# Performance work log

Measured on AMD Instinct MI355X. Metric: run time of the kernel, lower is better.

Reference implementation:

```python
import jax, jax.numpy as jnp
from jax import lax
import numpy as np

N, M, P, K = 2, 16384, 5023, 4
C_PLANE, HP = 32, 256
OUT_DIM = 32


def _harmonic(x):
    # pytorch3d HarmonicEmbedding(n=4, logspace, omega_0=1, append_input=True)
    f = jnp.asarray([1.0, 2.0, 4.0, 8.0], x.dtype)
    e = (x[..., None] * f).reshape(x.shape[:-1] + (-1,))  # [..., 12]
    return jnp.concatenate([jnp.sin(e), jnp.cos(e), x], axis=-1)  # [..., 27]


def _grid_sample2d(img, grid):
    # img [C,H,W], grid [M,2] (x->W, y->H) in [-1,1]; bilinear, zero pad, align_corners=False
    C, H, W = img.shape
    x = (grid[:, 0] + 1.0) * (W / 2.0) - 0.5
    y = (grid[:, 1] + 1.0) * (H / 2.0) - 0.5
    x0 = jnp.floor(x); y0 = jnp.floor(y)
    x1 = x0 + 1.0; y1 = y0 + 1.0
    wx1 = x - x0; wx0 = 1.0 - wx1
    wy1 = y - y0; wy0 = 1.0 - wy1
    def gather(ix, iy):
        valid = ((ix >= 0) & (ix < W) & (iy >= 0) & (iy < H)).astype(img.dtype)
        ixc = jnp.clip(ix, 0, W - 1).astype(jnp.int32)
        iyc = jnp.clip(iy, 0, H - 1).astype(jnp.int32)
        return img[:, iyc, ixc] * valid[None, :]  # [C,M]
    out = (gather(x0, y0) * (wx0 * wy0) + gather(x1, y0) * (wx1 * wy0)
           + gather(x0, y1) * (wx0 * wy1) + gather(x1, y1) * (wx1 * wy1))
    return out.T  # [M,C]


def _forward(coordinates, directions, points_position, tex_tplanes, emb_table,
             pw1, pb1, pw2, pb2, fw1, fb1, fw2, fb2, fw3, fb3, dw, db, rw1, rb1, rw2, rb2):
    c = coordinates
    p = points_position
    # --- triplane sampling (EG3D projections (x,y),(x,z),(z,x)), mean over planes ---
    proj = jnp.stack([c[..., :2],
                      c[..., jnp.array([0, 2])],
                      c[..., jnp.array([2, 0])]], axis=1)  # [N,3,M,2]
    tex = jax.vmap(jax.vmap(_grid_sample2d))(tex_tplanes, proj).mean(axis=1)  # [N,M,32]
    # --- KNN (squared distances, ascending, as pytorch3d knn_points) ---
    d2 = (jnp.sum(c * c, -1)[:, :, None] + jnp.sum(p * p, -1)[:, None, :]
          - 2.0 * jnp.einsum('nmc,npc->nmp', c, p))  # [N,M,P]
    negd, idx = lax.top_k(-d2, K)
    dist = -negd  # [N,M,K]
    nn = jax.vmap(lambda pts, i: pts[i])(p, idx)  # [N,M,K,3]
    pf = emb_table[idx]  # [N,M,K,32]
    rel = c[:, :, None, :] - nn
    rel = rel / jnp.maximum(jnp.linalg.norm(rel, axis=-1, keepdims=True), 1e-12)
    h = jnp.concatenate([pf, _harmonic(rel)], axis=-1)  # [N,M,K,59]
    h = jax.nn.relu(h @ pw1 + pb1) @ pw2 + pb2  # [N,M,K,32]
    w = 1.0 / dist
    w = w / jnp.sum(w, axis=1, keepdims=True)  # dim=1 exactly as in source
    pts_feat = jnp.sum(h * w[..., None], axis=2)  # [N,M,32]
    # --- dense MLP stack ---
    feat = jnp.concatenate([tex, pts_feat], axis=-1)  # [N,M,64]
    feat = jax.nn.relu(feat @ fw1 + fb1)
    feat = jax.nn.relu(feat @ fw2 + fb2)
    feat = feat @ fw3 + fb3  # [N,M,128]
    selector = jnp.all((c > -1.0) & (c < 1.0), axis=-1)  # [N,M]
    raw = (jax.nn.softplus(10.0 * (feat @ dw + db)) / 10.0) * selector[..., None]
    densities = 1.0 - jnp.exp(-raw)
    rays = directions / jnp.maximum(jnp.linalg.norm(directions, axis=-1, keepdims=True), 1e-12)
    rgb = jnp.concatenate([feat, _harmonic(rays)], axis=-1)  # [N,M,155]
    rgb = jax.nn.relu(rgb @ rw1 + rb1) @ rw2 + rb2  # [N,M,OUT_DIM]
    rgb = jnp.concatenate([jax.nn.sigmoid(rgb[..., :3]) * (1.0 + 2 * 0.001) - 0.001,
                           rgb[..., 3:]], axis=-1)
    return densities, rgb, dist


def setup_inputs() -> dict:
    key = jax.random.key(0)
    ks = jax.random.split(key, 16)
    rn = lambda k, s, sc=1.0: jax.random.normal(k, s, jnp.float32) * sc
    def lin(k, i, o):
        k1, k2 = jax.random.split(k)
        return rn(k1, (i, o), 1.0 / np.sqrt(i)), rn(k2, (o,), 0.01)
    coordinates = jax.random.uniform(ks[0], (N, M, 3), jnp.float32)
    directions = rn(ks[1], (N, M, 3))
    points_position = jax.random.uniform(ks[2], (N, P, 3), jnp.float32)
    tex_tplanes = rn(ks[3], (N, 3, C_PLANE, HP, HP))
    emb_table = rn(ks[4], (P, 32), 0.02)
    pw1, pb1 = lin(ks[5], 32 + 27, 64)
    pw2, pb2 = lin(ks[6], 64, 32)
    fw1, fb1 = lin(ks[7], 64, 128)
    fw2, fb2 = lin(ks[8], 128, 128)
    fw3, fb3 = lin(ks[9], 128, 128)
    dw, db = lin(ks[10], 128, 1)
    rw1, rb1 = lin(ks[11], 128 + 27, 64)
    rw2, rb2 = lin(ks[12], 64, OUT_DIM)
    return dict(coordinates=coordinates, directions=directions, points_position=points_position,
                tex_tplanes=tex_tplanes, emb_table=emb_table, pw1=pw1, pb1=pb1, pw2=pw2, pb2=pb2,
                fw1=fw1, fb1=fb1, fw2=fw2, fb2=fb2, fw3=fw3, fb3=fb3, dw=dw, db=db,
                rw1=rw1, rb1=rb1, rw2=rw2, rb2=rb2)


def reference(coordinates, directions, points_position, tex_tplanes, emb_table,
              pw1, pb1, pw2, pb2, fw1, fb1, fw2, fb2, fw3, fb3, dw, db, rw1, rb1, rw2, rb2):
    return _forward(coordinates, directions, points_position, tex_tplanes, emb_table,
                    pw1, pb1, pw2, pb2, fw1, fb1, fw2, fb2, fw3, fb3, dw, db, rw1, rb1, rw2, rb2)
```

## Files before the change

### kernel.cpp

```cpp
#include <hip/hip_runtime.h>
#include <float.h>
#include <math.h>

#define NB 2
#define MQ 16384
#define NQ (NB*MQ)
#define PP 5023
#define KNN 4
#define HPX 256
#define HWSZ (HPX*HPX)

#define OUT_RGB_OFF  ((size_t)NQ)
#define OUT_DIST_OFF ((size_t)NQ + (size_t)NQ*32)

#define WS_SUMS_OFF ((size_t)NQ*KNN*4)
#define WS_PTS4_OFF ((size_t)0x90000)
#define WS_WP_OFF   ((size_t)0xC0000)
#define WS_TEX_OFF  ((size_t)1<<20)

#define WP_PW1 0
#define WP_PW2 1920
#define WP_FW1 2944
#define WP_FW2 7040
#define WP_FW3 15232
#define WP_DW  23424
#define WP_RW1 23488
#define WP_RW2 28480

typedef __attribute__((ext_vector_type(2))) _Float16 half2v;

static __device__ __forceinline__ unsigned int pk2(float a, float b) {
    half2v h; h[0] = (_Float16)a; h[1] = (_Float16)b;
    return __builtin_bit_cast(unsigned int, h);
}
static __device__ __forceinline__ float2 upk(unsigned int u) {
    half2v h = __builtin_bit_cast(half2v, u);
    return make_float2((float)h[0], (float)h[1]);
}
static __device__ __forceinline__ float dot2(unsigned int a, unsigned int b, float c) {
    return __builtin_amdgcn_fdot2(__builtin_bit_cast(half2v, a),
                                  __builtin_bit_cast(half2v, b), c, false);
}

struct PackArgs {
    const float* src[8];
    int off[8]; int din[8]; int dout[8];
};
__global__ __launch_bounds__(256) void k_pack(PackArgs a, unsigned int* wp) {
    const int mid = blockIdx.y;
    const int idx = blockIdx.x * 256 + threadIdx.x;
    const int DIN = a.din[mid], DOUT = a.dout[mid];
    const int din2 = (DIN + 1) >> 1;
    if (idx >= din2 * DOUT) return;
    const int i2 = idx / DOUT, j = idx - i2 * DOUT;
    const float* s = a.src[mid];
    const float lo = s[(2*i2) * DOUT + j];
    const float hi = (2*i2 + 1 < DIN) ? s[(2*i2 + 1) * DOUT + j] : 0.f;
    wp[a.off[mid] + idx] = pk2(lo, hi);
}

__global__ __launch_bounds__(256) void k_pts4(const float* __restrict__ pts,
                                              float4* __restrict__ o) {
    const int i = blockIdx.x * 256 + threadIdx.x;
    if (i >= NB * PP) return;
    const float px = pts[3*i], py = pts[3*i+1], pz = pts[3*i+2];
    o[i] = make_float4(px, py, pz, fmaf(px, px, fmaf(py, py, pz*pz)));
}

__global__ __launch_bounds__(256) void k_transpose(const float* __restrict__ src,
                                                   float* __restrict__ dst) {
    const int tid = threadIdx.x;
    const int b = blockIdx.x;
    const int n3 = b >> 8;
    const int hw = ((b & 255) << 8) + tid;
    const float* s = src + (size_t)n3 * 32 * HWSZ + hw;
    float v[32];
#pragma unroll
    for (int c = 0; c < 32; ++c) v[c] = s[(size_t)c * HWSZ];
    float4* d = (float4*)(dst + ((size_t)n3 * HWSZ + hw) * 32);
#pragma unroll
    for (int c = 0; c < 8; ++c) d[c] = make_float4(v[4*c], v[4*c+1], v[4*c+2], v[4*c+3]);
}

__global__ __launch_bounds__(1024, 2) void k_knn(const float* __restrict__ coords,
                                                 const float4* __restrict__ pts4,
                                                 const float* __restrict__ pts,
                                                 float* __restrict__ odist,
                                                 int* __restrict__ oidx) {
    __shared__ unsigned int KB[16][4][64];
    const int tid  = threadIdx.x;
    const int lane = tid & 63;
    const int w    = __builtin_amdgcn_readfirstlane(tid >> 6);
    const int q0   = blockIdx.x * 64;
    const int q    = q0 + lane;
    const int n    = q0 >> 14;
    const float cx = coords[q*3+0], cy = coords[q*3+1], cz = coords[q*3+2];
    const float cc = fmaf(cx, cx, fmaf(cy, cy, cz*cz));
    const float4* __restrict__ p4 = pts4 + (size_t)n * PP;

    const int chunk  = (PP + 15) / 16;
    const int pstart = w * chunk;
    const int pend   = (pstart + chunk < PP) ? (pstart + chunk) : PP;

    unsigned int k0 = 0xFFFFFFFFu, k1 = 0xFFFFFFFFu, k2 = 0xFFFFFFFFu, k3 = 0xFFFFFFFFu;

#define INS(kb) { \
        unsigned int m2 = ((kb) > k2) ? (kb) : k2;  k3 = (k3 < m2) ? k3 : m2; \
        unsigned int m1 = ((kb) > k1) ? (kb) : k1;  k2 = (k2 < m1) ? k2 : m1; \
        unsigned int m0 = ((kb) > k0) ? (kb) : k0;  k1 = (k1 < m0) ? k1 : m0; \
        k0 = (k0 < (kb)) ? k0 : (kb); }

    int p = pstart;
    for (; p + 8 <= pend; p += 8) {
        float4 P[8];
#pragma unroll
        for (int j = 0; j < 8; ++j) P[j] = p4[p + j];
#pragma unroll
        for (int j = 0; j < 8; ++j) {
            const float dot = fmaf(cx, P[j].x, fmaf(cy, P[j].y, cz * P[j].z));
            float dd = fmaxf(fmaf(-2.0f, dot, cc + P[j].w), 0.f);
            const unsigned int kb = (__float_as_uint(dd) & 0xFFFFE000u) | (unsigned int)(p + j);
            INS(kb)
        }
    }
    for (; p < pend; ++p) {
        const float4 P = p4[p];
        const float dot = fmaf(cx, P.x, fmaf(cy, P.y, cz * P.z));
        float dd = fmaxf(fmaf(-2.0f, dot, cc + P.w), 0.f);
        const unsigned int kb = (__float_as_uint(dd) & 0xFFFFE000u) | (unsigned int)p;
        INS(kb)
    }

    KB[w][0][lane] = k0; KB[w][1][lane] = k1; KB[w][2][lane] = k2; KB[w][3][lane] = k3;
    __syncthreads();

    if (w == 0) {
        unsigned int s0 = 0xFFFFFFFFu, s1 = 0xFFFFFFFFu, s2 = 0xFFFFFFFFu, s3 = 0xFFFFFFFFu;
#pragma unroll
        for (int ww = 0; ww < 16; ++ww)
#pragma unroll
            for (int j = 0; j < 4; ++j) {
                const unsigned int kb = KB[ww][j][lane];
                unsigned int m2 = (kb > s2) ? kb : s2;  s3 = (s3 < m2) ? s3 : m2;
                unsigned int m1 = (kb > s1) ? kb : s1;  s2 = (s2 < m1) ? s2 : m1;
                unsigned int m0 = (kb > s0) ? kb : s0;  s1 = (s1 < m0) ? s1 : m0;
                s0 = (s0 < kb) ? s0 : kb;
            }
        const float* __restrict__ pb = pts + (size_t)n * PP * 3;
        int   id[4] = { (int)(s0 & 0x1FFFu), (int)(s1 & 0x1FFFu),
                        (int)(s2 & 0x1FFFu), (int)(s3 & 0x1FFFu) };
        float dv[4];
#pragma unroll
        for (int j = 0; j < 4; ++j) {
            const float px = pb[3*id[j]+0], py = pb[3*id[j]+1], pz = pb[3*id[j]+2];
            const float dt  = fmaf(cx, px, fmaf(cy, py, cz*pz));
            const float pp2 = fmaf(px, px, fmaf(py, py, pz*pz));
            dv[j] = fmaf(-2.0f, dt, cc + pp2);
        }
#define CSW(a,b) { bool sw = (dv[b] < dv[a]) || (dv[b] == dv[a] && id[b] < id[a]); \
                   if (sw) { float td=dv[a]; dv[a]=dv[b]; dv[b]=td; int ti=id[a]; id[a]=id[b]; id[b]=ti; } }
        CSW(0,1) CSW(2,3) CSW(0,2) CSW(1,3) CSW(1,2)
#undef CSW
        *(float4*)(odist + (size_t)q*4) = make_float4(dv[0], dv[1], dv[2], dv[3]);
        *(int4*)(oidx + (size_t)q*4)    = make_int4(id[0], id[1], id[2], id[3]);
    }
#undef INS
}

__global__ __launch_bounds__(1024) void k_sums(const float* __restrict__ dist,
                                               float* __restrict__ sums) {
    const int b = blockIdx.x;
    const int n = b >> 2, k = b & 3;
    float s = 0.f;
    for (int m = threadIdx.x; m < MQ; m += 1024)
        s += 1.0f / dist[((size_t)n * MQ + m) * 4 + k];
    __shared__ float red[1024];
    red[threadIdx.x] = s;
    __syncthreads();
    for (int off = 512; off > 0; off >>= 1) {
        if (threadIdx.x < off) red[threadIdx.x] += red[threadIdx.x + off];
        __syncthreads();
    }
    if (threadIdx.x == 0) sums[b] = red[0];
}

template<int DIN2, int DOUT, int TILE>
__device__ __forceinline__ void gemv_p(const unsigned int* __restrict__ Xp, int lane,
                                       const unsigned int* __restrict__ Wp,
                                       const float* __restrict__ bias,
                                       int j0, float (&acc)[TILE]) {
#pragma unroll
    for (int u = 0; u < TILE; ++u) acc[u] = bias[j0 + u];
#pragma unroll
    for (int i2 = 0; i2 < DIN2; ++i2) {
        const unsigned int xv = Xp[i2 * 64 + lane];
        const unsigned int* wr = Wp + i2 * DOUT + j0;
#pragma unroll
        for (int u = 0; u < TILE; ++u) acc[u] = dot2(xv, wr[u], acc[u]);
    }
}

static __device__ __forceinline__ float harm_val(int h, float rx, float ry, float rz) {
    if (h >= 27) return 0.f;
    float v;
    if (h < 24) {
        int base = (h < 12) ? h : (h - 12);
        float rv = (base >> 2) == 0 ? rx : ((base >> 2) == 1 ? ry : rz);
        float e = rv * (float)(1 << (base & 3));
        v = (h < 12) ? sinf(e) : cosf(e);
    } else {
        v = (h == 24) ? rx : ((h == 25) ? ry : rz);
    }
    return v;
}

__global__ __launch_bounds__(1024, 2) void k_main(
    const float* __restrict__ coords, const float* __restrict__ dirs,
    const float* __restrict__ pts, const float* __restrict__ tex_raw,
    const float* __restrict__ tex_t, const float* __restrict__ emb,
    const unsigned int* __restrict__ wp,
    const float* __restrict__ pb1, const float* __restrict__ pb2,
    const float* __restrict__ fb1, const float* __restrict__ fb2,
    const float* __restrict__ fb3, const float* __restrict__ db,
    const float* __restrict__ rb1, const float* __restrict__ rb2,
    const int* __restrict__ idxbuf, const float* __restrict__ distbuf,
    const float* __restrict__ sums, float* __restrict__ out, int use_tex_t)
{
    __shared__ unsigned int S[248 * 64];
    const int tid  = threadIdx.x;
    const int lane = tid & 63;
    const int wv   = __builtin_amdgcn_readfirstlane(tid >> 6);
    const int q0   = blockIdx.x * 64;
    const int n    = q0 >> 14;
    const int q    = q0 + lane;

    float tex_acc[2] = {0.f, 0.f};
    {
        const int g = wv;
        const float cx = coords[q*3+0], cy = coords[q*3+1], cz = coords[q*3+2];
#pragma unroll
        for (int pl = 0; pl < 3; ++pl) {
            float gx = (pl == 2) ? cz : cx;
            float gy = (pl == 0) ? cy : ((pl == 1) ? cz : cx);
            float x = (gx + 1.f) * 128.f - 0.5f;
            float y = (gy + 1.f) * 128.f - 0.5f;
            float x0f = floorf(x), y0f = floorf(y);
            float wx1 = x - x0f, wy1 = y - y0f;
            float wx0 = 1.f - wx1, wy0 = 1.f - wy1;
            int x0 = (int)x0f, y0 = (int)y0f;
            int n3 = n * 3 + pl;
            int  xs[4] = { x0, x0+1, x0,   x0+1 };
            int  ys[4] = { y0, y0,   y0+1, y0+1 };
            float wt[4] = { wx0*wy0, wx1*wy0, wx0*wy1, wx1*wy1 };
#pragma unroll
            for (int c = 0; c < 4; ++c) {
                int xi = xs[c], yi = ys[c];
                if (xi >= 0 && xi < HPX && yi >= 0 && yi < HPX) {
                    float wgt = wt[c];
                    if (use_tex_t) {
                        const float2 a = *(const float2*)(tex_t +
                            (((size_t)n3 * HWSZ + (size_t)yi * HPX + xi) * 32 + g * 2));
                        tex_acc[0] = fmaf(wgt, a.x, tex_acc[0]);
                        tex_acc[1] = fmaf(wgt, a.y, tex_acc[1]);
                    } else {
                        size_t base = ((size_t)(n3 * 32 + g * 2)) * HWSZ + (size_t)yi * HPX + xi;
                        tex_acc[0] = fmaf(wgt, tex_raw[base], tex_acc[0]);
                        tex_acc[1] = fmaf(wgt, tex_raw[base + HWSZ], tex_acc[1]);
                    }
                }
            }
        }
        tex_acc[0] *= (1.f / 3.f); tex_acc[1] *= (1.f / 3.f);
    }

    const int kk  = wv & 3;
    const int prt = wv >> 2;

    {
        const int id = idxbuf[(size_t)q*4 + kk];
        const int rb = kk * 30;
        if (prt < 2) {
#pragma unroll
            for (int t = 0; t < 2; ++t) {
                const float4 e = *(const float4*)(emb + (size_t)id * 32 + prt*16 + t*4 + 0)
                    , e2 = *(const float4*)(emb + (size_t)id * 32 + prt*16 + t*4 + 8);
                S[(rb + prt*8 + t*2    )*64 + lane] = pk2(e.x,  e.y);
                S[(rb + prt*8 + t*2 + 1)*64 + lane] = pk2(e.z,  e.w);
                S[(rb + prt*8 + t*2 + 4)*64 + lane] = pk2(e2.x, e2.y);
                S[(rb + prt*8 + t*2 + 5)*64 + lane] = pk2(e2.z, e2.w);
            }
        } else {
            const float cx = coords[q*3+0], cy = coords[q*3+1], cz = coords[q*3+2];
            const float nx = pts[((size_t)n*PP + id)*3 + 0];
            const float ny = pts[((size_t)n*PP + id)*3 + 1];
            const float nz = pts[((size_t)n*PP + id)*3 + 2];
            float rx = cx - nx, ry = cy - ny, rz = cz - nz;
            float nrm = sqrtf(fmaf(rx, rx, fmaf(ry, ry, rz*rz)));
            float inv = 1.f / fmaxf(nrm, 1e-12f);
            rx *= inv; ry *= inv; rz *= inv;
            const int pr0 = (prt == 2) ? 0 : 8;
            const int prn = (prt == 2) ? 8 : 6;
#pragma unroll
            for (int t = 0; t < 8; ++t) {
                if (t < prn) {
                    int pr = pr0 + t;
                    S[(rb + 16 + pr)*64 + lane] =
                        pk2(harm_val(2*pr, rx, ry, rz), harm_val(2*pr + 1, rx, ry, rz));
                }
            }
        }
    }
    __syncthreads();

    {
        float acc[16];
        gemv_p<30, 64, 16>(S + (kk*30)*64, lane, wp + WP_PW1, pb1, prt * 16, acc);
        const int rb = 120 + kk*32 + prt*8;
#pragma unroll
        for (int u = 0; u < 8; ++u)
            S[(rb + u)*64 + lane] = pk2(fmaxf(acc[2*u], 0.f), fmaxf(acc[2*u+1], 0.f));
    }
    __syncthreads();

    {
        float acc[8];
        gemv_p<32, 32, 8>(S + (120 + kk*32)*64, lane, wp + WP_PW2, pb2, prt * 8, acc);
        const float dist = distbuf[(size_t)q*4 + kk];
        const float wk = (1.0f / dist) / sums[n*4 + kk];
        const int rb = kk*16 + prt*4;
#pragma unroll
        for (int u = 0; u < 4; ++u)
            S[(rb + u)*64 + lane] = pk2(wk * acc[2*u], wk * acc[2*u+1]);
    }
    __syncthreads();

    {
        S[(128 + wv)*64 + lane] = pk2(tex_acc[0], tex_acc[1]);
        float a = 0.f, b = 0.f;
#pragma unroll
        for (int k = 0; k < 4; ++k) {
            float2 v = upk(S[(k*16 + wv)*64 + lane]);
            a += v.x; b += v.y;
        }
        S[(144 + wv)*64 + lane] = pk2(a, b);
    }
    __syncthreads();

    {
        float acc[8];
        gemv_p<32, 128, 8>(S + 128*64, lane, wp + WP_FW1, fb1, wv * 8, acc);
#pragma unroll
        for (int u = 0; u < 4; ++u)
            S[(4*wv + u)*64 + lane] = pk2(fmaxf(acc[2*u], 0.f), fmaxf(acc[2*u+1], 0.f));
    }
    __syncthreads();
    {
        float acc[8];
        gemv_p<64, 128, 8>(S, lane, wp + WP_FW2, fb2, wv * 8, acc);
#pragma unroll
        for (int u = 0; u < 4; ++u)
            S[(64 + 4*wv + u)*64 + lane] = pk2(fmaxf(acc[2*u], 0.f), fmaxf(acc[2*u+1], 0.f));
    }
    __syncthreads();
    {
        float acc[8];
        gemv_p<64, 128, 8>(S + 64*64, lane, wp + WP_FW3, fb3, wv * 8, acc);
#pragma unroll
        for (int u = 0; u < 4; ++u)
            S[(4*wv + u)*64 + lane] = pk2(acc[2*u], acc[2*u+1]);
    }
    __syncthreads();
    {
        if (wv < 14) {
            float dx = dirs[q*3+0], dy = dirs[q*3+1], dz = dirs[q*3+2];
            float dn = sqrtf(fmaf(dx, dx, fmaf(dy, dy, dz*dz)));
            float inv = 1.f / fmaxf(dn, 1e-12f);
            dx *= inv; dy *= inv; dz *= inv;
            S[(128 + wv)*64 + lane] = pk2(harm_val(2*wv, dx, dy, dz),
                                          harm_val(2*wv + 1, dx, dy, dz));
        } else if (wv == 15) {
            float z = db[0];
            const unsigned int* dwp = wp + WP_DW;
#pragma unroll
            for (int i2 = 0; i2 < 64; ++i2) z = dot2(S[i2*64 + lane], dwp[i2], z);
            const float cx = coords[q*3+0], cy = coords[q*3+1], cz = coords[q*3+2];
            float selv = (cx > -1.f && cx < 1.f && cy > -1.f && cy < 1.f &&
                          cz > -1.f && cz < 1.f) ? 1.f : 0.f;
            float t10 = 10.f * z;
            float sp = (t10 > 20.f) ? t10 : log1pf(expf(t10));
            float raw = sp * 0.1f * selv;
            out[q] = 1.f - expf(-raw);
        }
    }
    __syncthreads();
    {
        const int j0 = wv * 4;
        float acc[4];
        gemv_p<64, 64, 4>(S, lane, wp + WP_RW1, rb1, j0, acc);
#pragma unroll
        for (int t = 0; t < 14; ++t) {
            const unsigned int xv = S[(128 + t)*64 + lane];
            const unsigned int* wr = wp + WP_RW1 + (64 + t) * 64 + j0;
#pragma unroll
            for (int u = 0; u < 4; ++u) acc[u] = dot2(xv, wr[u], acc[u]);
        }
        S[(64 + 2*wv    )*64 + lane] = pk2(fmaxf(acc[0], 0.f), fmaxf(acc[1], 0.f));
        S[(64 + 2*wv + 1)*64 + lane] = pk2(fmaxf(acc[2], 0.f), fmaxf(acc[3], 0.f));
    }
    __syncthreads();
    {
        float acc[2];
        gemv_p<32, 32, 2>(S + 64*64, lane, wp + WP_RW2, rb2, wv * 2, acc);
#pragma unroll
        for (int u = 0; u < 2; ++u) {
            int j = wv*2 + u;
            float v = acc[u];
            if (j < 3) v = 1.002f * (1.f / (1.f + expf(-v))) - 0.001f;
            out[OUT_RGB_OFF + (size_t)q*32 + j] = v;
        }
    }
}

extern "C" void kernel_launch(void* const* d_in, const int* in_sizes, int n_in,
                              void* d_out, int out_size, void* d_ws, size_t ws_size,
                              hipStream_t stream) {
    (void)in_sizes; (void)n_in; (void)out_size;
    const float* coords = (const float*)d_in[0];
    const float* dirs   = (const float*)d_in[1];
    const float* pts    = (const float*)d_in[2];
    const float* tex    = (const float*)d_in[3];
    const float* emb    = (const float*)d_in[4];
    const float* pw1 = (const float*)d_in[5];  const float* pb1 = (const float*)d_in[6];
    const float* pw2 = (const float*)d_in[7];  const float* pb2 = (const float*)d_in[8];
    const float* fw1 = (const float*)d_in[9];  const float* fb1 = (const float*)d_in[10];
    const float* fw2 = (const float*)d_in[11]; const float* fb2 = (const float*)d_in[12];
    const float* fw3 = (const float*)d_in[13]; const float* fb3 = (const float*)d_in[14];
    const float* dw  = (const float*)d_in[15]; const float* db  = (const float*)d_in[16];
    const float* rw1 = (const float*)d_in[17]; const float* rb1 = (const float*)d_in[18];
    const float* rw2 = (const float*)d_in[19]; const float* rb2 = (const float*)d_in[20];

    float*        out    = (float*)d_out;
    int*          wsidx  = (int*)d_ws;
    float*        wssums = (float*)((char*)d_ws + WS_SUMS_OFF);
    float4*       wspts4 = (float4*)((char*)d_ws + WS_PTS4_OFF);
    unsigned int* wswp   = (unsigned int*)((char*)d_ws + WS_WP_OFF);
    float*        wstex  = (float*)((char*)d_ws + WS_TEX_OFF);

    const size_t need_tex = WS_TEX_OFF + (size_t)6 * HWSZ * 32 * 4;
    const int use_t = (ws_size >= need_tex) ? 1 : 0;

    PackArgs pa;
    pa.src[0] = pw1; pa.off[0] = WP_PW1; pa.din[0] = 59;  pa.dout[0] = 64;
    pa.src[1] = pw2; pa.off[1] = WP_PW2; pa.din[1] = 64;  pa.dout[1] = 32;
    pa.src[2] = fw1; pa.off[2] = WP_FW1; pa.din[2] = 64;  pa.dout[2] = 128;
    pa.src[3] = fw2; pa.off[3] = WP_FW2; pa.din[3] = 128; pa.dout[3] = 128;
    pa.src[4] = fw3; pa.off[4] = WP_FW3; pa.din[4] = 128; pa.dout[4] = 128;
    pa.src[5] = dw;  pa.off[5] = WP_DW;  pa.din[5] = 128; pa.dout[5] = 1;
    pa.src[6] = rw1; pa.off[6] = WP_RW1; pa.din[6] = 155; pa.dout[6] = 64;
    pa.src[7] = rw2; pa.off[7] = WP_RW2; pa.din[7] = 64;  pa.dout[7] = 32;

    k_pack<<<dim3(32, 8), 256, 0, stream>>>(pa, wswp);
    k_pts4<<<(NB*PP + 255)/256, 256, 0, stream>>>(pts, wspts4);
    if (use_t) k_transpose<<<6 * 256, 256, 0, stream>>>(tex, wstex);
    k_knn<<<NQ / 64, 1024, 0, stream>>>(coords, wspts4, pts, out + OUT_DIST_OFF, wsidx);
    k_sums<<<8, 1024, 0, stream>>>(out + OUT_DIST_OFF, wssums);
    k_main<<<NQ / 64, 1024, 0, stream>>>(coords, dirs, pts, tex, wstex, emb,
                                         wswp, pb1, pb2, fb1, fb2, fb3, db, rb1, rb2,
                                         wsidx, out + OUT_DIST_OFF, wssums, out, use_t);
}
```

Before: 330.4 us.

## Replace brute-force KNN with uniform-grid spatial hashing search

Builds a 12^3 uniform grid over the points with count, scan and scatter kernels, then searches expanding Chebyshev shells of cells per query with early termination. This replaces the exhaustive per-query scan of all points, which cuts distance evaluations. It also relaxes k_main launch bounds to one block per CU, removes readfirstlane on the wave index, and disables unroll on the density dot loop. Per-thread divergent loops and the shell stopping rule may hurt on clustered or out-of-cube queries and risk incorrect neighbours.

```diff
diff --git a/kernel.cpp b/kernel.cpp
--- a/kernel.cpp
+++ b/kernel.cpp
@@ -9,14 +9,20 @@
 #define KNN 4
 #define HPX 256
 #define HWSZ (HPX*HPX)
+#define GD 12
+#define GC (GD*GD*GD)
 
 #define OUT_RGB_OFF  ((size_t)NQ)
 #define OUT_DIST_OFF ((size_t)NQ + (size_t)NQ*32)
 
-#define WS_SUMS_OFF ((size_t)NQ*KNN*4)
-#define WS_PTS4_OFF ((size_t)0x90000)
-#define WS_WP_OFF   ((size_t)0xC0000)
-#define WS_TEX_OFF  ((size_t)1<<20)
+#define WS_SUMS_OFF   ((size_t)0x80000)
+#define WS_CNT_OFF    ((size_t)0x81000)
+#define WS_START_OFF  ((size_t)0x85000)
+#define WS_CURSOR_OFF ((size_t)0x89000)
+#define WS_PG_OFF     ((size_t)0x90000)
+#define WS_PID_OFF    ((size_t)0xB8000)
+#define WS_WP_OFF     ((size_t)0xC8000)
+#define WS_TEX_OFF    ((size_t)1<<20)
 
 #define WP_PW1 0
 #define WP_PW2 1920
@@ -40,6 +46,11 @@
 static __device__ __forceinline__ float dot2(unsigned int a, unsigned int b, float c) {
     return __builtin_amdgcn_fdot2(__builtin_bit_cast(half2v, a),
                                   __builtin_bit_cast(half2v, b), c, false);
+}
+
+static __device__ __forceinline__ int cell_of(float x) {
+    int g = (int)(x * (float)GD);
+    return (g < 0) ? 0 : ((g > GD-1) ? GD-1 : g);
 }
 
 struct PackArgs {
@@ -59,14 +70,6 @@
     wp[a.off[mid] + idx] = pk2(lo, hi);
 }
 
-__global__ __launch_bounds__(256) void k_pts4(const float* __restrict__ pts,
-                                              float4* __restrict__ o) {
-    const int i = blockIdx.x * 256 + threadIdx.x;
-    if (i >= NB * PP) return;
-    const float px = pts[3*i], py = pts[3*i+1], pz = pts[3*i+2];
-    o[i] = make_float4(px, py, pz, fmaf(px, px, fmaf(py, py, pz*pz)));
-}
-
 __global__ __launch_bounds__(256) void k_transpose(const float* __restrict__ src,
                                                    float* __restrict__ dst) {
     const int tid = threadIdx.x;
@@ -82,89 +85,117 @@
     for (int c = 0; c < 8; ++c) d[c] = make_float4(v[4*c], v[4*c+1], v[4*c+2], v[4*c+3]);
 }
 
-__global__ __launch_bounds__(1024, 2) void k_knn(const float* __restrict__ coords,
-                                                 const float4* __restrict__ pts4,
-                                                 const float* __restrict__ pts,
-                                                 float* __restrict__ odist,
-                                                 int* __restrict__ oidx) {
-    __shared__ unsigned int KB[16][4][64];
-    const int tid  = threadIdx.x;
-    const int lane = tid & 63;
-    const int w    = __builtin_amdgcn_readfirstlane(tid >> 6);
-    const int q0   = blockIdx.x * 64;
-    const int q    = q0 + lane;
-    const int n    = q0 >> 14;
+__global__ __launch_bounds__(256) void k_gcount(const float* __restrict__ pts,
+                                                unsigned int* __restrict__ cnt) {
+    const int i = blockIdx.x * 256 + threadIdx.x;
+    if (i >= NB * PP) return;
+    const int n = (i >= PP) ? 1 : 0;
+    const float px = pts[3*i], py = pts[3*i+1], pz = pts[3*i+2];
+    const int c = (cell_of(pz)*GD + cell_of(py))*GD + cell_of(px);
+    atomicAdd(&cnt[n*GC + c], 1u);
+}
+
+__global__ __launch_bounds__(1024) void k_gscan(const unsigned int* __restrict__ cnt,
+                                                unsigned int* __restrict__ start,
+                                                unsigned int* __restrict__ cursor) {
+    __shared__ unsigned int sc[1024];
+    const int t = threadIdx.x;
+#pragma unroll 1
+    for (int n = 0; n < 2; ++n) {
+        const unsigned int* c = cnt + n*GC;
+        unsigned int a = (2*t   < GC) ? c[2*t]   : 0u;
+        unsigned int b = (2*t+1 < GC) ? c[2*t+1] : 0u;
+        unsigned int s = a + b;
+        sc[t] = s;
+        __syncthreads();
+        for (int off = 1; off < 1024; off <<= 1) {
+            unsigned int v = (t >= off) ? sc[t - off] : 0u;
+            __syncthreads();
+            sc[t] += v;
+            __syncthreads();
+        }
+        unsigned int excl = sc[t] - s;
+        unsigned int base = n * PP;
+        if (2*t < GC)   { start[n*GC + 2*t]   = base + excl;
+                          cursor[n*GC + 2*t]  = base + excl; }
+        if (2*t+1 < GC) { start[n*GC + 2*t+1] = base + excl + a;
+                          cursor[n*GC + 2*t+1]= base + excl + a; }
+        __syncthreads();
+    }
+}
+
+__global__ __launch_bounds__(256) void k_gscatter(const float* __restrict__ pts,
+                                                  unsigned int* __restrict__ cursor,
+                                                  float4* __restrict__ pg,
+                                                  int* __restrict__ pid) {
+    const int i = blockIdx.x * 256 + threadIdx.x;
+    if (i >= NB * PP) return;
+    const int n = (i >= PP) ? 1 : 0;
+    const int local = i - n * PP;
+    const float px = pts[3*i], py = pts[3*i+1], pz = pts[3*i+2];
+    const int c = (cell_of(pz)*GD + cell_of(py))*GD + cell_of(px);
+    const unsigned int pos = atomicAdd(&cursor[n*GC + c], 1u);
+    pg[pos] = make_float4(px, py, pz, fmaf(px, px, fmaf(py, py, pz*pz)));
+    pid[pos] = local;
+}
+
+__global__ __launch_bounds__(256) void k_knn_grid(
+    const float* __restrict__ coords,
+    const unsigned int* __restrict__ cellStart,
+    const unsigned int* __restrict__ cellCnt,
+    const float4* __restrict__ pg, const int* __restrict__ pid,
+    float* __restrict__ odist, int* __restrict__ oidx)
+{
+    const int q = blockIdx.x * 256 + threadIdx.x;
+    const int n = q >> 14;
     const float cx = coords[q*3+0], cy = coords[q*3+1], cz = coords[q*3+2];
     const float cc = fmaf(cx, cx, fmaf(cy, cy, cz*cz));
-    const float4* __restrict__ p4 = pts4 + (size_t)n * PP;
-
-    const int chunk  = (PP + 15) / 16;
-    const int pstart = w * chunk;
-    const int pend   = (pstart + chunk < PP) ? (pstart + chunk) : PP;
-
-    unsigned int k0 = 0xFFFFFFFFu, k1 = 0xFFFFFFFFu, k2 = 0xFFFFFFFFu, k3 = 0xFFFFFFFFu;
-
-#define INS(kb) { \
-        unsigned int m2 = ((kb) > k2) ? (kb) : k2;  k3 = (k3 < m2) ? k3 : m2; \
-        unsigned int m1 = ((kb) > k1) ? (kb) : k1;  k2 = (k2 < m1) ? k2 : m1; \
-        unsigned int m0 = ((kb) > k0) ? (kb) : k0;  k1 = (k1 < m0) ? k1 : m0; \
-        k0 = (k0 < (kb)) ? k0 : (kb); }
-
-    int p = pstart;
-    for (; p + 8 <= pend; p += 8) {
-        float4 P[8];
-#pragma unroll
-        for (int j = 0; j < 8; ++j) P[j] = p4[p + j];
-#pragma unroll
-        for (int j = 0; j < 8; ++j) {
-            const float dot = fmaf(cx, P[j].x, fmaf(cy, P[j].y, cz * P[j].z));
-            float dd = fmaxf(fmaf(-2.0f, dot, cc + P[j].w), 0.f);
-            const unsigned int kb = (__float_as_uint(dd) & 0xFFFFE000u) | (unsigned int)(p + j);
-            INS(kb)
-        }
-    }
-    for (; p < pend; ++p) {
-        const float4 P = p4[p];
-        const float dot = fmaf(cx, P.x, fmaf(cy, P.y, cz * P.z));
-        float dd = fmaxf(fmaf(-2.0f, dot, cc + P.w), 0.f);
-        const unsigned int kb = (__float_as_uint(dd) & 0xFFFFE000u) | (unsigned int)p;
-        INS(kb)
-    }
-
-    KB[w][0][lane] = k0; KB[w][1][lane] = k1; KB[w][2][lane] = k2; KB[w][3][lane] = k3;
-    __syncthreads();
-
-    if (w == 0) {
-        unsigned int s0 = 0xFFFFFFFFu, s1 = 0xFFFFFFFFu, s2 = 0xFFFFFFFFu, s3 = 0xFFFFFFFFu;
-#pragma unroll
-        for (int ww = 0; ww < 16; ++ww)
-#pragma unroll
-            for (int j = 0; j < 4; ++j) {
-                const unsigned int kb = KB[ww][j][lane];
-                unsigned int m2 = (kb > s2) ? kb : s2;  s3 = (s3 < m2) ? s3 : m2;
-                unsigned int m1 = (kb > s1) ? kb : s1;  s2 = (s2 < m1) ? s2 : m1;
-                unsigned int m0 = (kb > s0) ? kb : s0;  s1 = (s1 < m0) ? s1 : m0;
-                s0 = (s0 < kb) ? s0 : kb;
+    const int cb = n * GC;
+    const int gx = cell_of(cx), gy = cell_of(cy), gz = cell_of(cz);
+    const float w = 1.0f / (float)GD;
+
+    float bd0 = FLT_MAX, bd1 = FLT_MAX, bd2 = FLT_MAX, bd3 = FLT_MAX;
+    int   bi0 = 0x7fffffff, bi1 = 0x7fffffff, bi2 = 0x7fffffff, bi3 = 0x7fffffff;
+
+#pragma unroll 1
+    for (int r = 0; r < GD; ++r) {
+        const int x0 = max(gx-r, 0), x1 = min(gx+r, GD-1);
+        const int y0 = max(gy-r, 0), y1 = min(gy+r, GD-1);
+        const int z0 = max(gz-r, 0), z1 = min(gz+r, GD-1);
+#pragma unroll 1
+        for (int zz = z0; zz <= z1; ++zz)
+#pragma unroll 1
+        for (int yy = y0; yy <= y1; ++yy)
+#pragma unroll 1
+        for (int xx = x0; xx <= x1; ++xx) {
+            const int chb = max(abs(xx-gx), max(abs(yy-gy), abs(zz-gz)));
+            if (chb != r) continue;
+            const int cid = cb + (zz*GD + yy)*GD + xx;
+            const unsigned int s = cellStart[cid];
+            const unsigned int e = s + cellCnt[cid];
+#pragma unroll 1
+            for (unsigned int j = s; j < e; ++j) {
+                const float4 P = pg[j];
+                const int i = pid[j];
+                const float dt = fmaf(cx, P.x, fmaf(cy, P.y, cz * P.z));
+                const float d = fmaf(-2.0f, dt, cc + P.w);
+                bool L3 = (d < bd3) || (d == bd3 && i < bi3);
+                bool L2 = (d < bd2) || (d == bd2 && i < bi2);
+                bool L1 = (d < bd1) || (d == bd1 && i < bi1);
+                bool L0 = (d < bd0) || (d == bd0 && i < bi0);
+                bd3 = L3 ? (L2 ? bd2 : d) : bd3;  bi3 = L3 ? (L2 ? bi2 : i) : bi3;
+                bd2 = L2 ? (L1 ? bd1 : d) : bd2;  bi2 = L2 ? (L1 ? bi1 : i) : bi2;
+                bd1 = L1 ? (L0 ? bd0 : d) : bd1;  bi1 = L1 ? (L0 ? bi0 : i) : bi1;
+                bd0 = L0 ? d : bd0;               bi0 = L0 ? i : bi0;
             }
-        const float* __restrict__ pb = pts + (size_t)n * PP * 3;
-        int   id[4] = { (int)(s0 & 0x1FFFu), (int)(s1 & 0x1FFFu),
-                        (int)(s2 & 0x1FFFu), (int)(s3 & 0x1FFFu) };
-        float dv[4];
-#pragma unroll
-        for (int j = 0; j < 4; ++j) {
-            const float px = pb[3*id[j]+0], py = pb[3*id[j]+1], pz = pb[3*id[j]+2];
-            const float dt  = fmaf(cx, px, fmaf(cy, py, cz*pz));
-            const float pp2 = fmaf(px, px, fmaf(py, py, pz*pz));
-            dv[j] = fmaf(-2.0f, dt, cc + pp2);
-        }
-#define CSW(a,b) { bool sw = (dv[b] < dv[a]) || (dv[b] == dv[a] && id[b] < id[a]); \
-                   if (sw) { float td=dv[a]; dv[a]=dv[b]; dv[b]=td; int ti=id[a]; id[a]=id[b]; id[b]=ti; } }
-        CSW(0,1) CSW(2,3) CSW(0,2) CSW(1,3) CSW(1,2)
-#undef CSW
-        *(float4*)(odist + (size_t)q*4) = make_float4(dv[0], dv[1], dv[2], dv[3]);
-        *(int4*)(oidx + (size_t)q*4)    = make_int4(id[0], id[1], id[2], id[3]);
-    }
-#undef INS
+        }
+        if (bd3 < FLT_MAX) {
+            const float rr = (float)r * w;
+            if (bd3 <= rr * rr * 0.9999f) break;
+        }
+    }
+    *(float4*)(odist + (size_t)q*4) = make_float4(bd0, bd1, bd2, bd3);
+    *(int4*)(oidx + (size_t)q*4)    = make_int4(bi0, bi1, bi2, bi3);
 }
 
 __global__ __launch_bounds__(1024) void k_sums(const float* __restrict__ dist,
@@ -214,7 +245,7 @@
     return v;
 }
 
-__global__ __launch_bounds__(1024, 2) void k_main(
+__global__ __launch_bounds__(1024, 1) void k_main(
     const float* __restrict__ coords, const float* __restrict__ dirs,
     const float* __restrict__ pts, const float* __restrict__ tex_raw,
     const float* __restrict__ tex_t, const float* __restrict__ emb,
@@ -229,7 +260,7 @@
     __shared__ unsigned int S[248 * 64];
     const int tid  = threadIdx.x;
     const int lane = tid & 63;
-    const int wv   = __builtin_amdgcn_readfirstlane(tid >> 6);
+    const int wv   = tid >> 6;
     const int q0   = blockIdx.x * 64;
     const int n    = q0 >> 14;
     const int q    = q0 + lane;
@@ -381,7 +412,7 @@
         } else if (wv == 15) {
             float z = db[0];
             const unsigned int* dwp = wp + WP_DW;
-#pragma unroll
+#pragma unroll 1
             for (int i2 = 0; i2 < 64; ++i2) z = dot2(S[i2*64 + lane], dwp[i2], z);
             const float cx = coords[q*3+0], cy = coords[q*3+1], cz = coords[q*3+2];
             float selv = (cx > -1.f && cx < 1.f && cy > -1.f && cy < 1.f &&
@@ -439,12 +470,16 @@
     const float* rw1 = (const float*)d_in[17]; const float* rb1 = (const float*)d_in[18];
     const float* rw2 = (const float*)d_in[19]; const float* rb2 = (const float*)d_in[20];
 
-    float*        out    = (float*)d_out;
-    int*          wsidx  = (int*)d_ws;
-    float*        wssums = (float*)((char*)d_ws + WS_SUMS_OFF);
-    float4*       wspts4 = (float4*)((char*)d_ws + WS_PTS4_OFF);
-    unsigned int* wswp   = (unsigned int*)((char*)d_ws + WS_WP_OFF);
-    float*        wstex  = (float*)((char*)d_ws + WS_TEX_OFF);
+    float*        out     = (float*)d_out;
+    int*          wsidx   = (int*)d_ws;
+    float*        wssums  = (float*)((char*)d_ws + WS_SUMS_OFF);
+    unsigned int* wscnt   = (unsigned int*)((char*)d_ws + WS_CNT_OFF);
+    unsigned int* wsstart = (unsigned int*)((char*)d_ws + WS_START_OFF);
+    unsigned int* wscur   = (unsigned int*)((char*)d_ws + WS_CURSOR_OFF);
+    float4*       wspg    = (float4*)((char*)d_ws + WS_PG_OFF);
+    int*          wspid   = (int*)((char*)d_ws + WS_PID_OFF);
+    unsigned int* wswp    = (unsigned int*)((char*)d_ws + WS_WP_OFF);
+    float*        wstex   = (float*)((char*)d_ws + WS_TEX_OFF);
 
     const size_t need_tex = WS_TEX_OFF + (size_t)6 * HWSZ * 32 * 4;
     const int use_t = (ws_size >= need_tex) ? 1 : 0;
@@ -459,10 +494,14 @@
     pa.src[6] = rw1; pa.off[6] = WP_RW1; pa.din[6] = 155; pa.dout[6] = 64;
     pa.src[7] = rw2; pa.off[7] = WP_RW2; pa.din[7] = 64;  pa.dout[7] = 32;
 
+    hipMemsetAsync(wscnt, 0, 2 * GC * sizeof(unsigned int), stream);
     k_pack<<<dim3(32, 8), 256, 0, stream>>>(pa, wswp);
-    k_pts4<<<(NB*PP + 255)/256, 256, 0, stream>>>(pts, wspts4);
     if (use_t) k_transpose<<<6 * 256, 256, 0, stream>>>(tex, wstex);
-    k_knn<<<NQ / 64, 1024, 0, stream>>>(coords, wspts4, pts, out + OUT_DIST_OFF, wsidx);
+    k_gcount<<<(NB*PP + 255)/256, 256, 0, stream>>>(pts, wscnt);
+    k_gscan<<<1, 1024, 0, stream>>>(wscnt, wsstart, wscur);
+    k_gscatter<<<(NB*PP + 255)/256, 256, 0, stream>>>(pts, wscur, wspg, wspid);
+    k_knn_grid<<<NQ / 256, 256, 0, stream>>>(coords, wsstart, wscnt, wspg, wspid,
+                                             out + OUT_DIST_OFF, wsidx);
     k_sums<<<8, 1024, 0, stream>>>(out + OUT_DIST_OFF, wssums);
     k_main<<<NQ / 64, 1024, 0, stream>>>(coords, dirs, pts, tex, wstex, emb,
                                          wswp, pb1, pb2, fb1, fb2, fb3, db, rb1, rb2,
```

After: 554.0 us. 1.68x slower.
